# Kernel optimization log

Measured on AMD Instinct MI355X. Metric: run time of the kernel, lower is better.

Reference implementation:

```python
import jax, jax.numpy as jnp
import numpy as np

HW = 8   # window height
WW = 8   # window width
NH = 8   # num heads
N = HW * WW  # tokens per window
DIM = 128
KEXPAND = 2


def _rel_index():
    # Swin relative-position index, [N, N] ints in [0, (2*HW-1)*(2*WW-1))
    coords = np.stack(np.meshgrid(np.arange(HW), np.arange(WW), indexing='ij')).reshape(2, -1)
    rel = (coords[:, :, None] - coords[:, None, :]).transpose(1, 2, 0)  # [N,N,2]
    rel[..., 0] += HW - 1
    rel[..., 1] += WW - 1
    rel[..., 0] *= 2 * WW - 1
    return jnp.asarray(rel.sum(-1))


def setup_inputs() -> dict:
    key = jax.random.key(0)
    ks = jax.random.split(key, 13)
    b, h, w, c = 4, 256, 256, DIM
    inp = {
        'qq': jax.random.normal(ks[0], (b, h * w, c), jnp.float32),
        'kk': jax.random.normal(ks[1], (b, h * w, KEXPAND * c), jnp.float32),
        'vv': jax.random.normal(ks[2], (b, h * w, c), jnp.float32),
        'w_q': jax.random.normal(ks[3], (c, c), jnp.float32) * 0.02,
        'b_q': jnp.zeros((c,), jnp.float32),
        'w_k': jax.random.normal(ks[4], (KEXPAND * c, c), jnp.float32) * 0.02,
        'b_k': jnp.zeros((c,), jnp.float32),
        'w_v': jax.random.normal(ks[5], (c, c), jnp.float32) * 0.02,
        'b_v': jnp.zeros((c,), jnp.float32),
        'w_o': jax.random.normal(ks[6], (c, c), jnp.float32) * 0.02,
        'b_o': jnp.zeros((c,), jnp.float32),
        'bias_table': jax.random.normal(ks[7], ((2 * HW - 1) * (2 * WW - 1), NH), jnp.float32) * 0.02,
        'h': h,
        'w': w,
    }
    return inp


def reference(qq, kk, vv, w_q, b_q, w_k, b_k, w_v, b_v, w_o, b_o, bias_table, h, w):
    b, n, c = qq.shape
    hd = c // NH
    pad_b = (-h) % HW
    pad_r = (-w) % WW
    Hp, Wp = h + pad_b, w + pad_r

    def pad_img(x):
        ck = x.shape[-1]
        x = x.reshape(b, h, w, ck)
        return jnp.pad(x, ((0, 0), (0, pad_b), (0, pad_r), (0, 0)))

    # QKV projections (zero-padded regions become just the bias, same as torch)
    qp = pad_img(qq) @ w_q + b_q  # [b, Hp, Wp, c]
    kp = pad_img(kk) @ w_k + b_k
    vp = pad_img(vv) @ w_v + b_v

    def windows(x):
        x = x.reshape(b, Hp // HW, HW, Wp // WW, WW, c)
        x = x.transpose(0, 1, 3, 2, 4, 5).reshape(-1, N, NH, hd)
        return x.transpose(0, 2, 1, 3)  # [nw, NH, N, hd]

    q, k, v = windows(qp), windows(kp), windows(vp)

    scores = jnp.einsum('wnqd,wnkd->wnqk', q, k) / jnp.sqrt(jnp.asarray(hd, q.dtype))
    bias = bias_table[_rel_index().reshape(-1)].reshape(N, N, NH).transpose(2, 0, 1)  # [NH,N,N]
    attn = jax.nn.softmax(scores + bias[None], axis=-1)
    y = jnp.einsum('wnqk,wnkd->wnqd', attn, v)  # [nw, NH, N, hd]

    # merge heads and un-window
    y = y.transpose(0, 2, 1, 3).reshape(b, Hp // HW, Wp // WW, HW, WW, c)
    y = y.transpose(0, 1, 3, 2, 4, 5).reshape(b, Hp, Wp, c)
    out = y @ w_o + b_o
    out = out[:, :h, :w, :]
    return out.reshape(b, -1, c)
```

## Files before the change

kernel.cpp:

```cpp
#include <hip/hip_runtime.h>
#include <cstdint>

typedef float f32x4  __attribute__((ext_vector_type(4)));
typedef float f32x16 __attribute__((ext_vector_type(16)));
typedef short bf16x8 __attribute__((ext_vector_type(8)));
typedef unsigned int u32;

#define QP_BASE 0
#define KP_BASE 16384
#define VT_BASE 32768

__device__ __forceinline__ unsigned short f2bf(float f){
  union { float f; uint32_t u; } v; v.f = f;
  uint32_t u = v.u;
  return (unsigned short)((u + 0x7FFFu + ((u >> 16) & 1u)) >> 16);
}
__device__ __forceinline__ float bf2f(unsigned short h){
  union { uint32_t u; float f; } v; v.u = ((uint32_t)h) << 16;
  return v.f;
}
__device__ __forceinline__ u32 pack2bf(float a, float b){
  return (u32)f2bf(a) | ((u32)f2bf(b) << 16);
}
__device__ __forceinline__ f32x4 mfma16(bf16x8 a, bf16x8 b, f32x4 c){
  return __builtin_amdgcn_mfma_f32_16x16x32_bf16(a, b, c, 0, 0, 0);
}
__device__ __forceinline__ f32x16 mfma32(bf16x8 a, bf16x8 b, f32x16 c){
  return __builtin_amdgcn_mfma_f32_32x32x16_bf16(a, b, c, 0, 0, 0);
}
__device__ __forceinline__ void gload_lds16(const void* gsrc, void* ldst){
  __builtin_amdgcn_global_load_lds(
    (const __attribute__((address_space(1))) unsigned int*)gsrc,
    (__attribute__((address_space(3))) unsigned int*)ldst, 16, 0, 0);
}

__global__ void prep_kernel(const float* __restrict__ wq, const float* __restrict__ wk,
                            const float* __restrict__ wv, const float* __restrict__ wo,
                            const float* __restrict__ btab, unsigned short* __restrict__ wsu)
{
  const int idx = blockIdx.x * 256 + threadIdx.x;
  if (idx < 16384){
    const int n = idx >> 7, k = idx & 127;
    wsu[n*128 + (k ^ ((n & 7) << 3))] = f2bf(wq[k*128 + n]);
  } else if (idx < 32768){
    const int i = idx - 16384, n = i >> 7, k = i & 127;
    wsu[16384 + n*128 + (k ^ ((n & 7) << 3))] = f2bf(wv[k*128 + n]);
  } else if (idx < 65536){
    const int i = idx - 32768, n = i >> 8, k = i & 255;
    wsu[32768 + n*256 + (k ^ ((n & 7) << 3))] = f2bf(wk[k*128 + n]);
  } else if (idx < 81920){
    const int i = idx - 65536, n = i >> 7, k = i & 127;
    const float f = wo[k*128 + n];
    const unsigned short hv = f2bf(f);
    wsu[65536 + n*128 + k] = hv;
    wsu[81920 + n*128 + k] = f2bf(f - bf2f(hv));
  } else if (idx < 98304){
    const int i = idx - 81920;
    const int q  = i & 31;
    const int ib = (i >> 5) & 7;
    const int h5 = (i >> 8) & 1;
    const int t  = (i >> 9) & 1;
    const int qh = (i >> 10) & 1;
    const int h  = (i >> 11);
    const int qg = qh*32 + q;
    const int qi = qg >> 3, qj = qg & 7;
    u32 wv2 = 0;
#pragma unroll
    for (int e = 0; e < 2; ++e){
      const int r = 2*ib + e;
      const int key = t*32 + 4*h5 + (r & 3) + 8*(r >> 2);
      const int ki = key >> 3, kj = key & 7;
      const int rel = (qi - ki + 7) * 15 + (qj - kj + 7);
      wv2 |= ((u32)f2bf(btab[rel*8 + h])) << (16*e);
    }
    reinterpret_cast<u32*>(wsu + 98304)[i] = wv2;
  }
}

template<int KC, int MODE>
__device__ __forceinline__ void proj_body(const float* __restrict__ X,
    const float* __restrict__ bias, const unsigned short* __restrict__ wbase_g,
    unsigned short* __restrict__ outg, char* smem, int w0, int nwin)
{
  constexpr int NKS = KC / 32;
  constexpr int SH  = (KC == 128) ? 8 : 9;
  constexpr int WBYTES = KC * 128 * 2;
  const int tid = threadIdx.x;
  const int wave = tid >> 6, lane = tid & 63;
  const int g = lane >> 4, c16 = lane & 15;

#pragma unroll
  for (int i = 0; i < WBYTES/4096; ++i)
    gload_lds16(reinterpret_cast<const char*>(wbase_g) + i*4096 + tid*16, smem + i*4096 + tid*16);
  __syncthreads();
  char* outstage = smem + WBYTES;

  float bias_r[8];
#pragma unroll
  for (int ct = 0; ct < 8; ++ct) bias_r[ct] = bias[ct*16 + c16];

  const int rA = 16*wave + c16;
  const int rowoff = ((rA >> 3) << 8) + (rA & 7);

  float4 raw[2*NKS];
  {
    const int win = w0;
    const long winbase = (long)(win >> 10)*65536 + (long)((win >> 5) & 31)*2048 + (win & 31)*8;
    const float* xrow = X + (winbase + rowoff) * KC;
#pragma unroll
    for (int ks = 0; ks < NKS; ++ks){
      const float4* p = reinterpret_cast<const float4*>(xrow + 32*ks + 8*g);
      raw[2*ks] = p[0]; raw[2*ks+1] = p[1];
    }
  }

  for (int wl = 0; wl < nwin; ++wl){
    const int win = w0 + wl;
    bf16x8 a[NKS];
#pragma unroll
    for (int ks = 0; ks < NKS; ++ks){
      const float4 x0 = raw[2*ks], x1 = raw[2*ks+1];
      bf16x8 t;
      t[0]=(short)f2bf(x0.x); t[1]=(short)f2bf(x0.y); t[2]=(short)f2bf(x0.z); t[3]=(short)f2bf(x0.w);
      t[4]=(short)f2bf(x1.x); t[5]=(short)f2bf(x1.y); t[6]=(short)f2bf(x1.z); t[7]=(short)f2bf(x1.w);
      a[ks] = t;
    }
    if (wl + 1 < nwin){
      const int win2 = win + 1;
      const long wb2 = (long)(win2 >> 10)*65536 + (long)((win2 >> 5) & 31)*2048 + (win2 & 31)*8;
      const float* xrow2 = X + (wb2 + rowoff) * KC;
#pragma unroll
      for (int ks = 0; ks < NKS; ++ks){
        const float4* p = reinterpret_cast<const float4*>(xrow2 + 32*ks + 8*g);
        raw[2*ks] = p[0]; raw[2*ks+1] = p[1];
      }
    }
    f32x4 acc[8];
#pragma unroll
    for (int ct = 0; ct < 8; ++ct) acc[ct] = f32x4{0.f,0.f,0.f,0.f};
#pragma unroll
    for (int ct = 0; ct < 8; ++ct){
      const int n = ct*16 + c16;
#pragma unroll
      for (int ks = 0; ks < NKS; ++ks){
        const bf16x8 b = *reinterpret_cast<const bf16x8*>(
            smem + ((n << SH) + (((32*ks + 8*g) << 1) ^ ((n & 7) << 4))));
        acc[ct] = mfma16(a[ks], b, acc[ct]);
      }
    }

    if (MODE == 0){
#pragma unroll
      for (int ct = 0; ct < 8; ++ct){
#pragma unroll
        for (int r = 0; r < 4; ++r){
          const int row = 16*wave + 4*g + r;
          const int off = (row << 8) + (((ct*16 + c16) << 1) ^ ((row & 15) << 4));
          *reinterpret_cast<unsigned short*>(outstage + off) = f2bf(acc[ct][r] + bias_r[ct]);
        }
      }
      asm volatile("s_waitcnt lgkmcnt(0)" ::: "memory");
      char* dst = reinterpret_cast<char*>(outg) + (size_t)win * 16384 + wave*4096;
      const char* srcs = outstage + wave*4096;
#pragma unroll
      for (int i = 0; i < 4; ++i){
        const uint4 d = *reinterpret_cast<const uint4*>(srcs + i*1024 + lane*16);
        *reinterpret_cast<uint4*>(dst + i*1024 + lane*16) = d;
      }
    } else {
#pragma unroll
      for (int ct = 0; ct < 8; ++ct){
#pragma unroll
        for (int r = 0; r < 4; ++r){
          const int key = 16*wave + 4*g + r;
          const int off = (ct << 11) + (c16 << 7) + ((key << 1) ^ ((c16 & 7) << 4));
          *reinterpret_cast<unsigned short*>(outstage + off) = f2bf(acc[ct][r] + bias_r[ct]);
        }
      }
      __syncthreads();
      char* dst = reinterpret_cast<char*>(outg) + (size_t)win * 16384;
#pragma unroll
      for (int i = 0; i < 4; ++i){
        const uint4 d = *reinterpret_cast<const uint4*>(outstage + tid*16 + i*4096);
        *reinterpret_cast<uint4*>(dst + tid*16 + i*4096) = d;
      }
      __syncthreads();
    }
  }
}

__global__ __launch_bounds__(256, 3) void proj_q(const float* __restrict__ qq,
    const float* __restrict__ b_q, const unsigned short* __restrict__ wsu,
    unsigned short* __restrict__ qs)
{
  __shared__ char smem[49152];
  proj_body<128,0>(qq, b_q, wsu, qs, smem, blockIdx.x*8, 8);
}
__global__ __launch_bounds__(256, 3) void proj_v(const float* __restrict__ vv,
    const float* __restrict__ b_v, const unsigned short* __restrict__ wsu,
    unsigned short* __restrict__ vsg)
{
  __shared__ char smem[49152];
  proj_body<128,2>(vv, b_v, wsu + 16384, vsg, smem, blockIdx.x*8, 8);
}
__global__ __launch_bounds__(256, 2) void proj_k(const float* __restrict__ kkin,
    const float* __restrict__ b_k, const unsigned short* __restrict__ wsu,
    unsigned short* __restrict__ ksg)
{
  __shared__ char smem[81920];
  proj_body<256,0>(kkin, b_k, wsu + 32768, ksg, smem, blockIdx.x*8, 8);
}

__global__ __launch_bounds__(512, 4) void attn_kernel(
    const unsigned short* __restrict__ qs, const unsigned short* __restrict__ ksg,
    const unsigned short* __restrict__ vsg, const unsigned short* __restrict__ wsu,
    const float* __restrict__ b_o, float* __restrict__ out)
{
  __shared__ char smem[49152];
  const int tid = threadIdx.x;
  const int wave = tid >> 6, lane = tid & 63;
  const int l31 = lane & 31, h5 = lane >> 5;
  const int qh = wave & 1, hp = wave >> 1;

  const int win = blockIdx.x;
  const int bb = win >> 10, wy = (win >> 5) & 31, wx = win & 31;
  const long winbase = (long)bb * 65536 + (long)wy * 2048 + wx * 8;

  const u32* bias_u = reinterpret_cast<const u32*>(wsu + 98304);

  {
    const char* srcs[3] = {
      reinterpret_cast<const char*>(qs)  + (size_t)win * 16384,
      reinterpret_cast<const char*>(ksg) + (size_t)win * 16384,
      reinterpret_cast<const char*>(vsg) + (size_t)win * 16384 };
#pragma unroll
    for (int rg = 0; rg < 3; ++rg)
#pragma unroll
      for (int j = 0; j < 2; ++j){
        const int off = j*8192 + tid*16;
        gload_lds16(srcs[rg] + off, smem + rg*16384 + off);
      }
  }
  __syncthreads();

  f32x16 y[2];
#pragma unroll
  for (int hh = 0; hh < 2; ++hh){
    const int h = 2*hp + hh;
    const int chb = (h*16 + 8*h5) * 2;
    bf16x8 kf0, kf1, qf;
    { const int row = l31;
      kf0 = *reinterpret_cast<const bf16x8*>(smem + KP_BASE + (row<<8) + (chb ^ ((row&15)<<4))); }
    { const int row = 32 + l31;
      kf1 = *reinterpret_cast<const bf16x8*>(smem + KP_BASE + (row<<8) + (chb ^ ((row&15)<<4))); }
    { const int row = qh*32 + l31;
      qf  = *reinterpret_cast<const bf16x8*>(smem + QP_BASE + (row<<8) + (chb ^ ((row&15)<<4))); }
    f32x16 z = {};
    f32x16 s0 = mfma32(kf0, qf, z);
    f32x16 s1 = mfma32(kf1, qf, z);

    const u32* bb2 = bias_u + ((((h*2 + qh)*2 + 0)*2 + h5)*8)*32 + l31;
    float t[32];
#pragma unroll
    for (int i = 0; i < 8; ++i){
      const u32 w0 = bb2[i*32];
      const u32 w1 = bb2[512 + i*32];
      t[2*i]     = fmaf(s0[2*i],   0.25f, bf2f((unsigned short)(w0 & 0xffff)));
      t[2*i+1]   = fmaf(s0[2*i+1], 0.25f, bf2f((unsigned short)(w0 >> 16)));
      t[16+2*i]  = fmaf(s1[2*i],   0.25f, bf2f((unsigned short)(w1 & 0xffff)));
      t[17+2*i]  = fmaf(s1[2*i+1], 0.25f, bf2f((unsigned short)(w1 >> 16)));
    }
    float m = t[0];
#pragma unroll
    for (int r = 1; r < 32; ++r) m = fmaxf(m, t[r]);
    m = fmaxf(m, __shfl_xor(m, 32));
    float sum = 0.f;
#pragma unroll
    for (int r = 0; r < 32; ++r){ t[r] = __expf(t[r] - m); sum += t[r]; }
    sum += __shfl_xor(sum, 32);
    const float rs = 1.0f / sum;
    u32 pk0[8], pk1[8];
#pragma unroll
    for (int i = 0; i < 8; ++i){
      pk0[i] = pack2bf(t[2*i]*rs,    t[2*i+1]*rs);
      pk1[i] = pack2bf(t[16+2*i]*rs, t[17+2*i]*rs);
    }

    f32x16 yy = {};
    const int chr = l31 & 15;
#pragma unroll
    for (int m4 = 0; m4 < 4; ++m4){
      const int jb = 4*(m4 & 1);
      const u32 a0 = (m4 < 2) ? pk0[jb]   : pk1[jb];
      const u32 a1 = (m4 < 2) ? pk0[jb+1] : pk1[jb+1];
      const u32 a2 = (m4 < 2) ? pk0[jb+2] : pk1[jb+2];
      const u32 a3 = (m4 < 2) ? pk0[jb+3] : pk1[jb+3];
      const u32 s0w = (u32)__shfl_xor((int)a0, 32);
      const u32 s1w = (u32)__shfl_xor((int)a1, 32);
      const u32 s2w = (u32)__shfl_xor((int)a2, 32);
      const u32 s3w = (u32)__shfl_xor((int)a3, 32);
      union { u32 w[4]; bf16x8 v; } afu;
      afu.w[0] = h5 ? s2w : a0;
      afu.w[1] = h5 ? s3w : a1;
      afu.w[2] = h5 ? a2  : s0w;
      afu.w[3] = h5 ? a3  : s1w;
      const int kb = 32*m4 + 16*h5;
      const bf16x8 bv = *reinterpret_cast<const bf16x8*>(
          smem + VT_BASE + (h<<11) + (chr<<7) + (kb ^ ((chr & 7) << 4)));
      yy = mfma32(afu.v, bv, yy);
    }
    y[hh] = yy;
  }
  __syncthreads();

  if (l31 < 16){
#pragma unroll
    for (int hh = 0; hh < 2; ++hh){
      const int ch = (2*hp + hh)*16 + l31;
#pragma unroll
      for (int r = 0; r < 16; ++r){
        const int row = qh*32 + (r & 3) + 8*(r >> 2) + 4*h5;
        const float v = y[hh][r];
        const unsigned short hv = f2bf(v);
        const unsigned short lv = f2bf(v - bf2f(hv));
        const int byte = (row << 8) + ((ch << 1) ^ ((row & 15) << 4));
        *reinterpret_cast<unsigned short*>(smem + byte)         = hv;
        *reinterpret_cast<unsigned short*>(smem + 16384 + byte) = lv;
      }
    }
  }
  __syncthreads();

  {
    const int g = lane >> 4, c16 = lane & 15;
    const int ct = wave;
    const unsigned short* WT_oh = wsu + 65536;
    const unsigned short* WT_ol = wsu + 81920;
    bf16x8 bh[4], bl[4];
#pragma unroll
    for (int ks = 0; ks < 4; ++ks){
      bh[ks] = *reinterpret_cast<const bf16x8*>(WT_oh + (ct*16+c16)*128 + 32*ks + 8*g);
      bl[ks] = *reinterpret_cast<const bf16x8*>(WT_ol + (ct*16+c16)*128 + 32*ks + 8*g);
    }
    const float bov = b_o[ct*16 + c16];
#pragma unroll
    for (int rt = 0; rt < 4; ++rt){
      const int row2 = rt*16 + c16;
      bf16x8 ah[4], al[4];
#pragma unroll
      for (int ks = 0; ks < 4; ++ks){
        const int byte = (row2 << 8) + ((64*ks + 16*g) ^ ((row2 & 15) << 4));
        ah[ks] = *reinterpret_cast<const bf16x8*>(smem + byte);
        al[ks] = *reinterpret_cast<const bf16x8*>(smem + 16384 + byte);
      }
      f32x4 acc = {};
#pragma unroll
      for (int ks = 0; ks < 4; ++ks){
        acc = mfma16(ah[ks], bh[ks], acc);
        acc = mfma16(al[ks], bh[ks], acc);
        acc = mfma16(ah[ks], bl[ks], acc);
      }
#pragma unroll
      for (int r = 0; r < 4; ++r){
        const int R = rt*16 + 4*g + r;
        const long tok = winbase + (long)(R >> 3)*256 + (R & 7);
        out[tok*128 + ct*16 + c16] = acc[r] + bov;
      }
    }
  }
}

extern "C" void kernel_launch(void* const* d_in, const int* in_sizes, int n_in,
                              void* d_out, int out_size, void* d_ws, size_t ws_size,
                              hipStream_t stream)
{
  (void)in_sizes; (void)n_in; (void)out_size; (void)ws_size;
  const float* qq   = (const float*)d_in[0];
  const float* kk   = (const float*)d_in[1];
  const float* vv   = (const float*)d_in[2];
  const float* w_q  = (const float*)d_in[3];
  const float* b_q  = (const float*)d_in[4];
  const float* w_k  = (const float*)d_in[5];
  const float* b_k  = (const float*)d_in[6];
  const float* w_v  = (const float*)d_in[7];
  const float* b_v  = (const float*)d_in[8];
  const float* w_o  = (const float*)d_in[9];
  const float* b_o  = (const float*)d_in[10];
  const float* btab = (const float*)d_in[11];
  unsigned short* wsu = (unsigned short*)d_ws;
  float* out = (float*)d_out;

  unsigned short* qsp = wsu + 131072;
  unsigned short* ksp = qsp + 33554432;
  unsigned short* vsp = ksp + 33554432;

  prep_kernel<<<384, 256, 0, stream>>>(w_q, w_k, w_v, w_o, btab, wsu);
  proj_q<<<512, 256, 0, stream>>>(qq, b_q, wsu, qsp);
  proj_v<<<512, 256, 0, stream>>>(vv, b_v, wsu, vsp);
  proj_k<<<512, 256, 0, stream>>>(kk, b_k, wsu, ksp);
  attn_kernel<<<4096, 512, 0, stream>>>(qsp, ksp, vsp, wsu, b_o, out);
}
```

Measured before the change: 274.2 us.

## Merge Q/K/V projection launches into one kernel and prefetch two windows ahead

The three projection kernels become a single launch, with each block choosing Q, V or K by blockIdx modulo 3. This removes two launch boundaries and lets the three projections run on the GPU concurrently. The projection body now keeps two register buffers of raw input and issues loads two windows ahead, so global-load latency is hidden over more compute. In exchange, every block declares 80KB of LDS and runs at occupancy 2, including the Q and V blocks that previously ran at 3. The extra prefetch buffer also adds register pressure.

```diff
diff --git a/kernel.cpp b/kernel.cpp
--- a/kernel.cpp
+++ b/kernel.cpp
@@ -102,19 +102,17 @@
   const int rA = 16*wave + c16;
   const int rowoff = ((rA >> 3) << 8) + (rA & 7);
 
-  float4 raw[2*NKS];
-  {
-    const int win = w0;
-    const long winbase = (long)(win >> 10)*65536 + (long)((win >> 5) & 31)*2048 + (win & 31)*8;
-    const float* xrow = X + (winbase + rowoff) * KC;
+  auto issue = [&](int win, float4 (&raw)[2*NKS]){
+    const long wb = (long)(win >> 10)*65536 + (long)((win >> 5) & 31)*2048 + (win & 31)*8;
+    const float* xrow = X + (wb + rowoff) * KC;
 #pragma unroll
     for (int ks = 0; ks < NKS; ++ks){
       const float4* p = reinterpret_cast<const float4*>(xrow + 32*ks + 8*g);
       raw[2*ks] = p[0]; raw[2*ks+1] = p[1];
     }
-  }
-
-  for (int wl = 0; wl < nwin; ++wl){
+  };
+
+  auto step = [&](int wl, float4 (&raw)[2*NKS]){
     const int win = w0 + wl;
     bf16x8 a[NKS];
 #pragma unroll
@@ -125,16 +123,7 @@
       t[4]=(short)f2bf(x1.x); t[5]=(short)f2bf(x1.y); t[6]=(short)f2bf(x1.z); t[7]=(short)f2bf(x1.w);
       a[ks] = t;
     }
-    if (wl + 1 < nwin){
-      const int win2 = win + 1;
-      const long wb2 = (long)(win2 >> 10)*65536 + (long)((win2 >> 5) & 31)*2048 + (win2 & 31)*8;
-      const float* xrow2 = X + (wb2 + rowoff) * KC;
-#pragma unroll
-      for (int ks = 0; ks < NKS; ++ks){
-        const float4* p = reinterpret_cast<const float4*>(xrow2 + 32*ks + 8*g);
-        raw[2*ks] = p[0]; raw[2*ks+1] = p[1];
-      }
-    }
+    if (wl + 2 < nwin) issue(win + 2, raw);
     f32x4 acc[8];
 #pragma unroll
     for (int ct = 0; ct < 8; ++ct) acc[ct] = f32x4{0.f,0.f,0.f,0.f};
@@ -186,29 +175,29 @@
       }
       __syncthreads();
     }
-  }
-}
-
-__global__ __launch_bounds__(256, 3) void proj_q(const float* __restrict__ qq,
-    const float* __restrict__ b_q, const unsigned short* __restrict__ wsu,
-    unsigned short* __restrict__ qs)
-{
-  __shared__ char smem[49152];
-  proj_body<128,0>(qq, b_q, wsu, qs, smem, blockIdx.x*8, 8);
-}
-__global__ __launch_bounds__(256, 3) void proj_v(const float* __restrict__ vv,
-    const float* __restrict__ b_v, const unsigned short* __restrict__ wsu,
-    unsigned short* __restrict__ vsg)
-{
-  __shared__ char smem[49152];
-  proj_body<128,2>(vv, b_v, wsu + 16384, vsg, smem, blockIdx.x*8, 8);
-}
-__global__ __launch_bounds__(256, 2) void proj_k(const float* __restrict__ kkin,
-    const float* __restrict__ b_k, const unsigned short* __restrict__ wsu,
-    unsigned short* __restrict__ ksg)
+  };
+
+  float4 rawA[2*NKS], rawB[2*NKS];
+  issue(w0, rawA);
+  issue(w0 + 1, rawB);
+  for (int wl = 0; wl < nwin; wl += 2){
+    step(wl, rawA);
+    step(wl + 1, rawB);
+  }
+}
+
+__global__ __launch_bounds__(256, 2) void proj_all(
+    const float* __restrict__ qq, const float* __restrict__ kkin, const float* __restrict__ vvin,
+    const float* __restrict__ b_q, const float* __restrict__ b_k, const float* __restrict__ b_v,
+    const unsigned short* __restrict__ wsu,
+    unsigned short* __restrict__ qs, unsigned short* __restrict__ ksg, unsigned short* __restrict__ vsg)
 {
   __shared__ char smem[81920];
-  proj_body<256,0>(kkin, b_k, wsu + 32768, ksg, smem, blockIdx.x*8, 8);
+  const int type = blockIdx.x % 3;
+  const int w0 = (blockIdx.x / 3) * 8;
+  if (type == 0)      proj_body<128,0>(qq,   b_q, wsu,         qs,  smem, w0, 8);
+  else if (type == 1) proj_body<128,2>(vvin, b_v, wsu + 16384, vsg, smem, w0, 8);
+  else                proj_body<256,0>(kkin, b_k, wsu + 32768, ksg, smem, w0, 8);
 }
 
 __global__ __launch_bounds__(512, 4) void attn_kernel(
@@ -395,8 +384,6 @@
   unsigned short* vsp = ksp + 33554432;
 
   prep_kernel<<<384, 256, 0, stream>>>(w_q, w_k, w_v, w_o, btab, wsu);
-  proj_q<<<512, 256, 0, stream>>>(qq, b_q, wsu, qsp);
-  proj_v<<<512, 256, 0, stream>>>(vv, b_v, wsu, vsp);
-  proj_k<<<512, 256, 0, stream>>>(kk, b_k, wsu, ksp);
+  proj_all<<<1536, 256, 0, stream>>>(qq, kk, vv, b_q, b_k, b_v, wsu, qsp, ksp, vsp);
   attn_kernel<<<4096, 512, 0, stream>>>(qsp, ksp, vsp, wsu, b_o, out);
 }
```

Result: no change. 272.8 us (-0.5%).
